# Performance work log

Measured on AMD Instinct MI355X. Metric: run time of the kernel, lower is better.

The kernel has to match this reference:

```python
import jax, jax.numpy as jnp
import numpy as np

E = 8            # num_experts
K = 2            # num_experts_per_tok
D = 1024         # n_embd
BLOCK = 64       # block_size
D_FFN = ((4 * D // K) + BLOCK - 1) // BLOCK * BLOCK  # 2048
B, S = 4, 2048
T = B * S
CAP = T * K + E * BLOCK  # fixed upper bound on total padded tokens


def setup_inputs() -> dict:
    key = jax.random.key(0)
    k1, k2, k3 = jax.random.split(key, 3)
    x = jax.random.normal(k1, (B, S, D), dtype=jnp.float32)
    w_router = jax.random.normal(k2, (E, D), dtype=jnp.float32) * 0.02
    w1 = jax.random.normal(k3, (D, D_FFN * E), dtype=jnp.float32) * 0.02
    return {"x": x, "w_router": w_router, "w1": w1}


def reference(x, w_router, w1):
    x_flat = x.reshape(-1, D)                                  # [T, D]
    # --- route ---
    logits = x_flat @ w_router.T                               # [T, E]
    probs = jax.nn.softmax(logits.astype(jnp.float32), axis=-1)
    topv, sel = jax.lax.top_k(probs, K)                        # [T, K]
    topv = topv / topv.sum(axis=-1, keepdims=True)             # norm_topk_prob
    topv = topv.astype(x.dtype)                                # (unused by this truncated forward)
    # --- sort replicated tokens by expert (stable) ---
    e_flat = sel.reshape(-1)                                   # [T*K]
    order = jnp.argsort(e_flat, stable=True)                   # [T*K]
    es = e_flat[order]                                         # sorted expert ids
    counts = jax.ops.segment_sum(jnp.ones_like(e_flat), e_flat, num_segments=E)  # tokens/expert
    gs = (counts + BLOCK - 1) // BLOCK * BLOCK                 # padded tokens/expert
    cum_o = jnp.concatenate([jnp.zeros(1, counts.dtype), jnp.cumsum(counts)])  # [E+1]
    cum_p = jnp.concatenate([jnp.zeros(1, gs.dtype), jnp.cumsum(gs)])          # [E+1]
    # destination row of each sorted token in the padded buffer
    rank_in_expert = jnp.arange(T * K) - cum_o[es]
    dst = cum_p[es] + rank_in_expert                           # [T*K]
    # x_rep = repeat_interleave(x_flat, K); x_sorted = x_rep[order] = x_flat[order // K]
    x_padded = jnp.zeros((CAP, D), x.dtype).at[dst].set(x_flat[order // K])
    # --- grouped GEMM: each padded row hits its expert's w1 slice ---
    w1_r = w1.reshape(D, E, D_FFN)
    rows = jnp.arange(CAP)
    out = jnp.zeros((CAP, D_FFN), x.dtype)
    for e in range(E):
        mask = ((rows >= cum_p[e]) & (rows < cum_p[e + 1]))[:, None].astype(x.dtype)
        out = out + (x_padded * mask) @ w1_r[:, e, :]
    return out  # [CAP, D_FFN]; rows beyond total_padded_tokens are exactly zero
```

## Files before the change

kernel.cpp:

```cpp
#include <hip/hip_runtime.h>
#include <stdint.h>

#define E_       8
#define D_       1024
#define DFFN_    2048
#define T_       8192
#define TK_      16384
#define CAP_     16896
#define MAXT_    144

#define WS_SEL      0u
#define WS_TOTALS   0x10200u
#define WS_TILES    0x11300u
#define WS_ROWSRC   0x12000u
#define WS_XBF      0x23000u
#define WS_W1T      (0x23000u + 34603008u)

typedef __bf16 bf16x8 __attribute__((ext_vector_type(8)));
typedef float  f32x4  __attribute__((ext_vector_type(4)));

__device__ __forceinline__ unsigned short f2bf(float f) {
  union { float f; uint32_t u; } v; v.f = f;
  return (unsigned short)((v.u + 0x7fffu + ((v.u >> 16) & 1u)) >> 16);
}

__global__ __launch_bounds__(256) void k_rw(const float* __restrict__ x,
                                            const float* __restrict__ wr,
                                            const float* __restrict__ w1,
                                            int* __restrict__ sel,
                                            unsigned short* __restrict__ xbf,
                                            unsigned short* __restrict__ w1t,
                                            float* __restrict__ out) {
  __shared__ __align__(16) unsigned char smem[33024];
  int tid = threadIdx.x;
  int bx = blockIdx.x;

  if (bx >= 1536) {
    int row = TK_ + (bx - 1536);
    float4 z = {0.f, 0.f, 0.f, 0.f};
    float4* o = (float4*)(out + (size_t)row * DFFN_);
    o[tid] = z;
    o[tid + 256] = z;
    return;
  }

  if (bx < 512) {
    float* lwr = (float*)smem;
    for (int i = tid; i < E_ * D_ / 4; i += 256)
      ((float4*)lwr)[i] = ((const float4*)wr)[i];
    __syncthreads();
    int wave = tid >> 6, lane = tid & 63;

    for (int tk = 0; tk < 4; ++tk) {
      int t = bx * 16 + wave * 4 + tk;
      double acc[E_];
#pragma unroll
      for (int e = 0; e < E_; ++e) acc[e] = 0.0;
      const float4* xr = (const float4*)(x + (size_t)t * D_);
      ushort4* xw = (ushort4*)(xbf + (size_t)t * D_);
#pragma unroll
      for (int j = 0; j < 4; ++j) {
        float4 v = xr[j * 64 + lane];
        ushort4 o;
        o.x = f2bf(v.x); o.y = f2bf(v.y); o.z = f2bf(v.z); o.w = f2bf(v.w);
        xw[j * 64 + lane] = o;
        int dbase = j * 256 + lane * 4;
#pragma unroll
        for (int e = 0; e < E_; ++e) {
          float4 w = *(const float4*)(lwr + e * D_ + dbase);
          acc[e] += (double)v.x * w.x + (double)v.y * w.y +
                    (double)v.z * w.z + (double)v.w * w.w;
        }
      }
#pragma unroll
      for (int e = 0; e < E_; ++e) {
        acc[e] += __shfl_xor(acc[e], 1, 64);
        acc[e] += __shfl_xor(acc[e], 2, 64);
        acc[e] += __shfl_xor(acc[e], 4, 64);
      }
      double s01 = (lane & 1) ? acc[1] : acc[0];
      double s23 = (lane & 1) ? acc[3] : acc[2];
      double s45 = (lane & 1) ? acc[5] : acc[4];
      double s67 = (lane & 1) ? acc[7] : acc[6];
      double t0 = (lane & 2) ? s23 : s01;
      double t1 = (lane & 2) ? s67 : s45;
      double u  = (lane & 4) ? t1 : t0;
      u += __shfl_xor(u, 8, 64);
      u += __shfl_xor(u, 16, 64);
      u += __shfl_xor(u, 32, 64);
      double lg[E_];
#pragma unroll
      for (int e = 0; e < E_; ++e) lg[e] = __shfl(u, e, 64);
      int e1 = 0; double b1 = lg[0];
#pragma unroll
      for (int e = 1; e < E_; ++e) if (lg[e] > b1) { b1 = lg[e]; e1 = e; }
      int e2 = (e1 == 0) ? 1 : 0; double b2 = lg[e2];
#pragma unroll
      for (int e = 0; e < E_; ++e) if (e != e1 && lg[e] > b2) { b2 = lg[e]; e2 = e; }
      if (lane == 0) {
        sel[2 * t]     = e1;
        sel[2 * t + 1] = e2;
      }
    }
  } else {
    typedef unsigned short row258[258];
    row258* lds = (row258*)smem;
    int b = bx - 512;
    int n0 = (b & 63) * 256, d0 = (b >> 6) * 64;
    int rIn = tid >> 6, c4 = tid & 63;
#pragma unroll
    for (int p = 0; p < 16; ++p) {
      int row = p * 4 + rIn;
      float4 v = *(const float4*)(w1 + (size_t)(d0 + row) * 16384 + n0 + c4 * 4);
      lds[row][c4 * 4 + 0] = f2bf(v.x);
      lds[row][c4 * 4 + 1] = f2bf(v.y);
      lds[row][c4 * 4 + 2] = f2bf(v.z);
      lds[row][c4 * 4 + 3] = f2bf(v.w);
    }
    __syncthreads();
    int d2 = (tid & 15) * 4, nn = tid >> 4;
#pragma unroll
    for (int q = 0; q < 16; ++q) {
      int n = q * 16 + nn;
      ushort4 o;
      o.x = lds[d2 + 0][n]; o.y = lds[d2 + 1][n];
      o.z = lds[d2 + 2][n]; o.w = lds[d2 + 3][n];
      *(ushort4*)(w1t + (size_t)(n0 + n) * 1024 + d0 + d2) = o;
    }
  }
}

__global__ __launch_bounds__(1024) void k_sort(const int* __restrict__ sel,
                                               int* __restrict__ totals,
                                               int* __restrict__ tiles,
                                               int* __restrict__ row_src) {
  __shared__ int spanCnt[1024][9];
  __shared__ int spanOff[1024][9];
  __shared__ int chunkOff[64][8];
  __shared__ int scnt[8];
  __shared__ int scum[9];
  __shared__ int lsel[16384];
  int t = threadIdx.x;
  int base = t * 16;

#pragma unroll
  for (int e = 0; e < 8; ++e) spanCnt[t][e] = 0;
#pragma unroll
  for (int j = 0; j < 16; ++j) {
    int e = sel[base + j];
    lsel[base + j] = e;
    spanCnt[t][e] += 1;
  }
  __syncthreads();

  if (t < 512) {
    int c = t >> 3, e = t & 7;
    int run = 0;
#pragma unroll
    for (int s = 0; s < 16; ++s) {
      spanOff[c * 16 + s][e] = run;
      run += spanCnt[c * 16 + s][e];
    }
    chunkOff[c][e] = run;
  }
  __syncthreads();

  if (t < 8) {
    int run = 0;
    for (int c = 0; c < 64; ++c) {
      int v = chunkOff[c][t];
      chunkOff[c][t] = run;
      run += v;
    }
    scnt[t] = run;
  }
  __syncthreads();

  if (t == 0) {
    int cp = 0, nt = 0;
    scum[0] = 0;
    for (int e = 0; e < E_; ++e) {
      int cnt = scnt[e];
      int gs = (cnt + 63) / 64 * 64;
      int r = 0;
      while (r < gs) {
        int m = (gs - r >= 128) ? 128 : 64;
        int mv = cnt - r;
        if (mv < 0) mv = 0;
        if (mv > m) mv = m;
        tiles[nt++] = (cp + r) | (e << 15) | ((m == 128) ? (1 << 18) : 0) | (mv << 19);
        r += m;
      }
      cp += gs;
      scum[e + 1] = cp;
    }
    totals[0] = cp;
    totals[1] = nt;
  }
  __syncthreads();

  for (int e = 0; e < E_; ++e) {
    int s = scum[e] + scnt[e], en = scum[e + 1];
    for (int i = s + t; i < en; i += 1024) row_src[i] = -1;
  }
  for (int i = scum[8] + t; i < CAP_ + 64; i += 1024) row_src[i] = -1;

#pragma unroll
  for (int e = 0; e < 8; ++e) spanCnt[t][e] = 0;
#pragma unroll
  for (int j = 0; j < 16; ++j) {
    int e = lsel[base + j];
    int dst = scum[e] + chunkOff[t >> 4][e] + spanOff[t][e] + spanCnt[t][e];
    spanCnt[t][e] += 1;
    row_src[dst] = (base + j) >> 1;
  }
}

#define READ_A(dst, KS)                                                         \
  {                                                                             \
    const unsigned short* p_ = As + (wr * 64 + lane15) * 64;                    \
    int co_ = (((KS) * 64 + g16) ^ swz) >> 1;                                   \
    _Pragma("unroll") for (int mi = 0; mi < 4; ++mi)                            \
      dst[mi] = *(const bf16x8*)(p_ + mi * 1024 + co_);                         \
  }

#define READ_B(dst, KS)                                                         \
  {                                                                             \
    const unsigned short* p_ = Bs + (wc * 64 + lane15) * 64;                    \
    int co_ = (((KS) * 64 + g16) ^ swz) >> 1;                                   \
    _Pragma("unroll") for (int ni = 0; ni < 4; ++ni)                            \
      dst[ni] = *(const bf16x8*)(p_ + ni * 1024 + co_);                         \
  }

#define MFMA16(AV, BV)                                                          \
  __builtin_amdgcn_s_setprio(1);                                                \
  _Pragma("unroll") for (int mi = 0; mi < 4; ++mi)                              \
    _Pragma("unroll") for (int ni = 0; ni < 4; ++ni)                            \
      acc[mi][ni] = __builtin_amdgcn_mfma_f32_16x16x32_bf16(                    \
          AV[mi], BV[ni], acc[mi][ni], 0, 0, 0);                                \
  __builtin_amdgcn_s_setprio(0);

__global__ __launch_bounds__(256, 4) void k_gemm(const unsigned short* __restrict__ xbf,
                                                 const unsigned short* __restrict__ w1t,
                                                 const int* __restrict__ row_src,
                                                 const int* __restrict__ tiles,
                                                 const int* __restrict__ totals,
                                                 float* __restrict__ out) {
  int P = blockIdx.y * MAXT_ + blockIdx.x;
  int L = (P & 7) * (MAXT_ * 16 / 8) + (P >> 3);
  int mtile = L >> 4, ny = L & 15;
  if (mtile >= totals[1]) return;

  int info = tiles[mtile];
  int rowBase = info & 0x7FFF;
  int e = (info >> 15) & 7;
  int mLimit = ((info >> 18) & 1) ? 128 : 64;
  int mValid = (info >> 19) & 0x1FF;

  __shared__ unsigned short As[128 * 64];
  __shared__ unsigned short Bs[128 * 64];

  int tid = threadIdx.x, wave = tid >> 6, lane = tid & 63;
  int lane15 = lane & 15;
  int g16 = (lane >> 4) * 16;
  int swz = (lane15 & 7) << 4;
  int wr = wave >> 1, wc = wave & 1;

  int rr = tid >> 3;
  int co = ((tid & 7) ^ (rr & 7)) << 3;
  int woff = (tid >> 6) << 9;

  const unsigned short* Asrc[4];
#pragma unroll
  for (int q = 0; q < 4; ++q) {
    int sr = row_src[rowBase + q * 32 + rr];
    if ((unsigned)sr >= (unsigned)T_) sr = 0;
    Asrc[q] = xbf + (size_t)sr * D_ + co;
  }
  const unsigned short* Bg = w1t + ((size_t)e * DFFN_ + (size_t)ny * 128) * D_;

  f32x4 acc[4][4];
#pragma unroll
  for (int i = 0; i < 4; ++i)
#pragma unroll
    for (int j = 0; j < 4; ++j) acc[i][j] = (f32x4){0.f, 0.f, 0.f, 0.f};

  for (int t = 0; t < 16; ++t) {
    int k0 = t * 64;
#pragma unroll
    for (int q = 0; q < 4; ++q)
      __builtin_amdgcn_global_load_lds(
          (const __attribute__((address_space(1))) void*)(Asrc[q] + k0),
          (__attribute__((address_space(3))) void*)(As + q * 2048 + woff), 16, 0, 0);
#pragma unroll
    for (int q = 0; q < 4; ++q)
      __builtin_amdgcn_global_load_lds(
          (const __attribute__((address_space(1))) void*)(Bg + (size_t)(q * 32 + rr) * D_ + k0 + co),
          (__attribute__((address_space(3))) void*)(Bs + q * 2048 + woff), 16, 0, 0);
    __syncthreads();

    bf16x8 a0[4], b0[4], a1[4], b1[4];
    READ_A(a0, 0);
    READ_B(b0, 0);
    MFMA16(a0, b0);
    READ_A(a1, 1);
    READ_B(b1, 1);
    MFMA16(a1, b1);
    __syncthreads();
  }

#pragma unroll
  for (int mi = 0; mi < 4; ++mi) {
    int mrow = wr * 64 + mi * 16;
    if (mrow >= mLimit) continue;
    int rbase = mrow + (lane >> 4) * 4;
#pragma unroll
    for (int ni = 0; ni < 4; ++ni) {
      int col = ny * 128 + wc * 64 + ni * 16 + lane15;
      f32x4 v = acc[mi][ni];
#pragma unroll
      for (int q = 0; q < 4; ++q) {
        float val = (rbase + q < mValid) ? v[q] : 0.0f;
        out[(size_t)(rowBase + rbase + q) * DFFN_ + col] = val;
      }
    }
  }
}

extern "C" void kernel_launch(void* const* d_in, const int* in_sizes, int n_in,
                              void* d_out, int out_size, void* d_ws, size_t ws_size,
                              hipStream_t stream) {
  const float* x  = (const float*)d_in[0];
  const float* wr = (const float*)d_in[1];
  const float* w1 = (const float*)d_in[2];
  float* out = (float*)d_out;
  char* ws = (char*)d_ws;

  int* sel     = (int*)(ws + WS_SEL);
  int* totals  = (int*)(ws + WS_TOTALS);
  int* tiles   = (int*)(ws + WS_TILES);
  int* row_src = (int*)(ws + WS_ROWSRC);
  unsigned short* xbf = (unsigned short*)(ws + WS_XBF);
  unsigned short* w1t = (unsigned short*)(ws + WS_W1T);

  k_rw<<<2048, 256, 0, stream>>>(x, wr, w1, sel, xbf, w1t, out);
  k_sort<<<1, 1024, 0, stream>>>(sel, totals, tiles, row_src);
  k_gemm<<<dim3(MAXT_, 16), 256, 0, stream>>>(xbf, w1t, row_src, tiles, totals, out);
}
```

Before: 156.8 us.

## Parallelize expert sort using per-block histograms from routing kernel

The routing kernel now writes a per-block expert histogram alongside the top-2 selections. The single-block sort is replaced by a 65-block placement kernel. Each block prefix-sums the histograms, and 64 blocks scatter rows using ballot/popcount ranks while the last block builds the tile list and fills padding. This removes the serial single-workgroup bottleneck between routing and GEMM, at the cost of redundant prefix computation in every block and an extra workspace buffer.

Result: faster. 126.6 us (median of 2 runs) (-19.2%).

```diff
diff --git a/kernel.cpp b/kernel.cpp
--- a/kernel.cpp
+++ b/kernel.cpp
@@ -15,6 +15,7 @@
 #define WS_ROWSRC   0x12000u
 #define WS_XBF      0x23000u
 #define WS_W1T      (0x23000u + 34603008u)
+#define WS_H        (0x23000u + 34603008u + 33554432u)
 
 typedef __bf16 bf16x8 __attribute__((ext_vector_type(8)));
 typedef float  f32x4  __attribute__((ext_vector_type(4)));
@@ -28,6 +29,7 @@
                                             const float* __restrict__ wr,
                                             const float* __restrict__ w1,
                                             int* __restrict__ sel,
+                                            int* __restrict__ h,
                                             unsigned short* __restrict__ xbf,
                                             unsigned short* __restrict__ w1t,
                                             float* __restrict__ out) {
@@ -46,6 +48,7 @@
 
   if (bx < 512) {
     float* lwr = (float*)smem;
+    int* selL = (int*)(smem + 32768);
     for (int i = tid; i < E_ * D_ / 4; i += 256)
       ((float4*)lwr)[i] = ((const float4*)wr)[i];
     __syncthreads();
@@ -100,7 +103,16 @@
       if (lane == 0) {
         sel[2 * t]     = e1;
         sel[2 * t + 1] = e2;
-      }
+        selL[wave * 8 + tk * 2]     = e1;
+        selL[wave * 8 + tk * 2 + 1] = e2;
+      }
+    }
+    __syncthreads();
+    if (tid < E_) {
+      int c = 0;
+#pragma unroll
+      for (int i = 0; i < 32; ++i) c += (selL[i] == tid);
+      h[bx * E_ + tid] = c;
     }
   } else {
     typedef unsigned short row258[258];
@@ -130,89 +142,91 @@
   }
 }
 
-__global__ __launch_bounds__(1024) void k_sort(const int* __restrict__ sel,
+__global__ __launch_bounds__(256) void k_place(const int* __restrict__ sel,
+                                               const int* __restrict__ h,
                                                int* __restrict__ totals,
                                                int* __restrict__ tiles,
                                                int* __restrict__ row_src) {
-  __shared__ int spanCnt[1024][9];
-  __shared__ int spanOff[1024][9];
-  __shared__ int chunkOff[64][8];
+  __shared__ int hL[512][8];
+  __shared__ int preSC[64][8];
   __shared__ int scnt[8];
   __shared__ int scum[9];
-  __shared__ int lsel[16384];
-  int t = threadIdx.x;
-  int base = t * 16;
-
-#pragma unroll
-  for (int e = 0; e < 8; ++e) spanCnt[t][e] = 0;
-#pragma unroll
-  for (int j = 0; j < 16; ++j) {
-    int e = sel[base + j];
-    lsel[base + j] = e;
-    spanCnt[t][e] += 1;
-  }
+  int tid = threadIdx.x;
+  int c = blockIdx.x;
+
+  for (int i = tid; i < 512 * 8 / 4; i += 256)
+    ((int4*)&hL[0][0])[i] = ((const int4*)h)[i];
   __syncthreads();
 
-  if (t < 512) {
-    int c = t >> 3, e = t & 7;
+  for (int idx = tid; idx < 512; idx += 256) {
+    int sc = idx >> 3, e = idx & 7;
+    int s = 0;
+#pragma unroll
+    for (int i = 0; i < 8; ++i) s += hL[sc * 8 + i][e];
+    preSC[sc][e] = s;
+  }
+  __syncthreads();
+
+  if (tid < 8) {
     int run = 0;
-#pragma unroll
-    for (int s = 0; s < 16; ++s) {
-      spanOff[c * 16 + s][e] = run;
-      run += spanCnt[c * 16 + s][e];
-    }
-    chunkOff[c][e] = run;
+    for (int sc = 0; sc < 64; ++sc) {
+      int v = preSC[sc][tid];
+      preSC[sc][tid] = run;
+      run += v;
+    }
+    scnt[tid] = run;
   }
   __syncthreads();
-
-  if (t < 8) {
-    int run = 0;
-    for (int c = 0; c < 64; ++c) {
-      int v = chunkOff[c][t];
-      chunkOff[c][t] = run;
-      run += v;
-    }
-    scnt[t] = run;
-  }
-  __syncthreads();
-
-  if (t == 0) {
-    int cp = 0, nt = 0;
+  if (tid == 0) {
+    int cp = 0;
     scum[0] = 0;
     for (int e = 0; e < E_; ++e) {
-      int cnt = scnt[e];
-      int gs = (cnt + 63) / 64 * 64;
-      int r = 0;
-      while (r < gs) {
-        int m = (gs - r >= 128) ? 128 : 64;
-        int mv = cnt - r;
-        if (mv < 0) mv = 0;
-        if (mv > m) mv = m;
-        tiles[nt++] = (cp + r) | (e << 15) | ((m == 128) ? (1 << 18) : 0) | (mv << 19);
-        r += m;
-      }
-      cp += gs;
+      cp += (scnt[e] + 63) / 64 * 64;
       scum[e + 1] = cp;
     }
-    totals[0] = cp;
-    totals[1] = nt;
   }
   __syncthreads();
 
-  for (int e = 0; e < E_; ++e) {
-    int s = scum[e] + scnt[e], en = scum[e + 1];
-    for (int i = s + t; i < en; i += 1024) row_src[i] = -1;
-  }
-  for (int i = scum[8] + t; i < CAP_ + 64; i += 1024) row_src[i] = -1;
-
-#pragma unroll
-  for (int e = 0; e < 8; ++e) spanCnt[t][e] = 0;
-#pragma unroll
-  for (int j = 0; j < 16; ++j) {
-    int e = lsel[base + j];
-    int dst = scum[e] + chunkOff[t >> 4][e] + spanOff[t][e] + spanCnt[t][e];
-    spanCnt[t][e] += 1;
-    row_src[dst] = (base + j) >> 1;
+  if (c < 64) {
+    int j = tid;
+    int e = sel[c * 256 + j];
+    int w = j >> 6;
+    int partial = 0;
+    for (int i = 0; i < 2 * w; ++i) partial += hL[c * 8 + i][e];
+    unsigned long long below = ((1ULL << (j & 63)) - 1ULL);
+    int rank = 0;
+#pragma unroll
+    for (int ee = 0; ee < 8; ++ee) {
+      unsigned long long m = __ballot(e == ee);
+      if (ee == e) rank = __popcll(m & below);
+    }
+    int dst = scum[e] + preSC[c][e] + partial + rank;
+    row_src[dst] = (c * 256 + j) >> 1;
+  } else {
+    if (tid == 0) {
+      int nt = 0;
+      for (int e = 0; e < E_; ++e) {
+        int cnt = scnt[e];
+        int cp = scum[e];
+        int gs = scum[e + 1] - cp;
+        int r = 0;
+        while (r < gs) {
+          int m = (gs - r >= 128) ? 128 : 64;
+          int mv = cnt - r;
+          if (mv < 0) mv = 0;
+          if (mv > m) mv = m;
+          tiles[nt++] = (cp + r) | (e << 15) | ((m == 128) ? (1 << 18) : 0) | (mv << 19);
+          r += m;
+        }
+      }
+      totals[0] = scum[8];
+      totals[1] = nt;
+    }
+    for (int e = 0; e < E_; ++e) {
+      int s = scum[e] + scnt[e], en = scum[e + 1];
+      for (int i = s + tid; i < en; i += 256) row_src[i] = -1;
+    }
+    for (int i = scum[8] + tid; i < CAP_ + 64; i += 256) row_src[i] = -1;
   }
 }
 
@@ -340,10 +354,11 @@
   int* totals  = (int*)(ws + WS_TOTALS);
   int* tiles   = (int*)(ws + WS_TILES);
   int* row_src = (int*)(ws + WS_ROWSRC);
+  int* h       = (int*)(ws + WS_H);
   unsigned short* xbf = (unsigned short*)(ws + WS_XBF);
   unsigned short* w1t = (unsigned short*)(ws + WS_W1T);
 
-  k_rw<<<2048, 256, 0, stream>>>(x, wr, w1, sel, xbf, w1t, out);
-  k_sort<<<1, 1024, 0, stream>>>(sel, totals, tiles, row_src);
+  k_rw<<<2048, 256, 0, stream>>>(x, wr, w1, sel, h, xbf, w1t, out);
+  k_place<<<65, 256, 0, stream>>>(sel, h, totals, tiles, row_src);
   k_gemm<<<dim3(MAXT_, 16), 256, 0, stream>>>(xbf, w1t, row_src, tiles, totals, out);
 }
```
